# Performance work log

Hardware: AMD Instinct MI355X
Metric: run time of the kernel (lower is better)

Reference implementation:

```python
import jax, jax.numpy as jnp
import numpy as np

EPS = 1e-8  # torch CosineSimilarity eps


def _l2_normalize(x):
    n = jnp.sqrt(jnp.sum(x * x, axis=-1, keepdims=True))
    return x / jnp.maximum(n, EPS)


def setup_inputs() -> dict:
    key = jax.random.key(0)
    k1, k2, k3 = jax.random.split(key, 3)
    B, D, K = 4096, 1024, 256
    datapoints = jax.random.normal(k1, (B, D), dtype=jnp.float32)
    centroid = jax.random.normal(k2, (K, D), dtype=jnp.float32)
    batch_cos_sim = jax.random.normal(k3, (B, B), dtype=jnp.float32)
    return {"datapoints": datapoints, "centroid": centroid, "batch_cos_sim": batch_cos_sim}


def reference(datapoints, centroid, batch_cos_sim):
    # --- _clustering: cosine similarity datapoints[B,D] vs centroid[K,D] (temp=1) ---
    dn = _l2_normalize(datapoints)                       # [B, D]
    cn = _l2_normalize(centroid)                         # [K, D]
    intra_cos_sim = jnp.einsum('bd,kd->bk', dn, cn)      # [B, K]
    dp_index = jnp.argmax(intra_cos_sim, axis=-1)        # [B]

    # --- _intra_class_adjacency: one-hot matmul, zero diagonal ---
    onehot = jax.nn.one_hot(dp_index, centroid.shape[0], dtype=jnp.float32)  # [B, K]
    dp_cluster = jnp.einsum('bk,ck->bc', onehot, onehot)                      # [B, B]
    B = datapoints.shape[0]
    dp_cluster = dp_cluster * (1.0 - jnp.eye(B, dtype=dp_cluster.dtype))
    index_dp = onehot.T.astype(jnp.int32)                # [K, B]

    # --- gather centroid each datapoint belongs to ---
    dp_centroid = centroid[dp_index]                     # [B, D]

    # --- provide_hard_negative: top-2, take 2nd-best centroid ---
    top_vals, top_idx = jax.lax.top_k(intra_cos_sim, 2)  # [B, 2]
    hard_neg_index = top_idx[:, 1]                       # [B]
    hard_negative = centroid[hard_neg_index]             # [B, D]

    return (intra_cos_sim, dp_index, dp_cluster, index_dp, dp_centroid,
            hard_negative, hard_neg_index, top_vals[:, 1])
```

## Files before the change

kernel.cpp:

```cpp
#include <hip/hip_runtime.h>
#include <hip/hip_bf16.h>
#include <math.h>

#define B_N 4096
#define D_N 1024
#define K_N 256
#define NSTEP 32

typedef __attribute__((ext_vector_type(8))) short bf16x8;
typedef __attribute__((ext_vector_type(8))) unsigned short u16x8;
typedef __attribute__((ext_vector_type(4))) float f32x4;
typedef __attribute__((ext_vector_type(4))) float f32x4v;
typedef __attribute__((ext_vector_type(4))) int   i32x4;

static constexpr float K_EPS = 1e-8f;

static __device__ __forceinline__ unsigned short f32_to_bf16_rne(float f) {
    unsigned x = __builtin_bit_cast(unsigned, f);
    unsigned r = (x + 0x7FFFu + ((x >> 16) & 1u)) >> 16;
    return (unsigned short)r;
}
static __device__ __forceinline__ float bf16_bits_to_f32(unsigned short h) {
    unsigned x = ((unsigned)h) << 16;
    return __builtin_bit_cast(float, x);
}
static __device__ __forceinline__ void cvt8(
    float e0, float e1, float e2, float e3,
    float e4, float e5, float e6, float e7, u16x8& hv, u16x8& lv)
{
    ushort h0=f32_to_bf16_rne(e0), h1=f32_to_bf16_rne(e1),
           h2=f32_to_bf16_rne(e2), h3=f32_to_bf16_rne(e3),
           h4=f32_to_bf16_rne(e4), h5=f32_to_bf16_rne(e5),
           h6=f32_to_bf16_rne(e6), h7=f32_to_bf16_rne(e7);
    hv = (u16x8){h0,h1,h2,h3,h4,h5,h6,h7};
    lv = (u16x8){f32_to_bf16_rne(e0 - bf16_bits_to_f32(h0)),
                 f32_to_bf16_rne(e1 - bf16_bits_to_f32(h1)),
                 f32_to_bf16_rne(e2 - bf16_bits_to_f32(h2)),
                 f32_to_bf16_rne(e3 - bf16_bits_to_f32(h3)),
                 f32_to_bf16_rne(e4 - bf16_bits_to_f32(h4)),
                 f32_to_bf16_rne(e5 - bf16_bits_to_f32(h5)),
                 f32_to_bf16_rne(e6 - bf16_bits_to_f32(h6)),
                 f32_to_bf16_rne(e7 - bf16_bits_to_f32(h7))};
}

__global__ __launch_bounds__(256) void kcent_kernel(
    const float* __restrict__ cent,
    ushort* __restrict__ phi, ushort* __restrict__ plo)
{
    int n   = blockIdx.x;
    int tid = threadIdx.x;
    float4 v = reinterpret_cast<const float4*>(cent + (size_t)n * D_N)[tid];
    float s = v.x * v.x + v.y * v.y + v.z * v.z + v.w * v.w;
    #pragma unroll
    for (int o = 32; o > 0; o >>= 1) s += __shfl_down(s, o);
    __shared__ float red[4];
    __shared__ float s_inv;
    if ((tid & 63) == 0) red[tid >> 6] = s;
    __syncthreads();
    if (tid == 0) {
        float t = red[0] + red[1] + red[2] + red[3];
        s_inv = 1.0f / fmaxf(sqrtf(t), K_EPS);
    }
    __syncthreads();
    float inv = s_inv;
    float e[4] = {v.x * inv, v.y * inv, v.z * inv, v.w * inv};
    ushort h4[4], l4[4];
    #pragma unroll
    for (int j = 0; j < 4; ++j) {
        ushort h = f32_to_bf16_rne(e[j]);
        float lo = e[j] - bf16_bits_to_f32(h);
        h4[j] = h;
        l4[j] = f32_to_bf16_rne(lo);
    }
    int nt = n >> 4, lr = n & 15;
    int k8 = tid >> 1, half = tid & 1;
    int t  = k8 >> 2, lg = k8 & 3;
    size_t chunk = (size_t)(nt * 32 + t) * 64 + lg * 16 + lr;
    *reinterpret_cast<ushort4*>(phi + chunk * 8 + half * 4) =
        make_ushort4(h4[0], h4[1], h4[2], h4[3]);
    *reinterpret_cast<ushort4*>(plo + chunk * 8 + half * 4) =
        make_ushort4(l4[0], l4[1], l4[2], l4[3]);
}

__global__ __launch_bounds__(1024) void kmain_kernel(
    const float* __restrict__ dp, const float* __restrict__ cent,
    const ushort* __restrict__ phi, const ushort* __restrict__ plo,
    float* __restrict__ out_sims, float* __restrict__ out_dpidx,
    float* __restrict__ out_hnidx, float* __restrict__ out_top1,
    float* __restrict__ out_dpcent, float* __restrict__ out_hneg,
    int* __restrict__ ws_dpidx)
{
    __shared__ ushort AhL[16 * 1024];
    __shared__ ushort AlL[16 * 1024];
    __shared__ float  simsL[16 * 256];
    int tid  = threadIdx.x;
    int lane = tid & 63;
    int w    = tid >> 6;
    int lr   = lane & 15;
    int lg   = lane >> 4;
    int brow = blockIdx.x * 16;

    const ushort* bh = phi + (size_t)w * 32 * 512 + (size_t)lane * 8;
    const ushort* bl = plo + (size_t)w * 32 * 512 + (size_t)lane * 8;

    #define LBF(t, H, L)                                                  \
        H = *reinterpret_cast<const bf16x8*>(bh + (size_t)(t) * 512);     \
        L = *reinterpret_cast<const bf16x8*>(bl + (size_t)(t) * 512);

    bf16x8 h0,l0,h1,l1,h2,l2,h3,l3,h4,l4,h5,l5,h6,l6,h7,l7;
    LBF(0,h0,l0) LBF(1,h1,l1) LBF(2,h2,l2) LBF(3,h3,l3)
    LBF(4,h4,l4) LBF(5,h5,l5) LBF(6,h6,l6) LBF(7,h7,l7)

    {
        const f32x4v* r4 = reinterpret_cast<const f32x4v*>(
            dp + (size_t)(brow + w) * D_N);
        f32x4v a0 = __builtin_nontemporal_load(r4 + lane*4+0);
        f32x4v a1 = __builtin_nontemporal_load(r4 + lane*4+1);
        f32x4v a2 = __builtin_nontemporal_load(r4 + lane*4+2);
        f32x4v a3 = __builtin_nontemporal_load(r4 + lane*4+3);
        float s = a0[0]*a0[0] + a0[1]*a0[1] + a0[2]*a0[2] + a0[3]*a0[3]
                + a1[0]*a1[0] + a1[1]*a1[1] + a1[2]*a1[2] + a1[3]*a1[3]
                + a2[0]*a2[0] + a2[1]*a2[1] + a2[2]*a2[2] + a2[3]*a2[3]
                + a3[0]*a3[0] + a3[1]*a3[1] + a3[2]*a3[2] + a3[3]*a3[3];
        #pragma unroll
        for (int o = 1; o < 64; o <<= 1) s += __shfl_xor(s, o);
        float inv = 1.0f / fmaxf(sqrtf(s), K_EPS);
        u16x8 hv, lv;
        cvt8(a0[0]*inv, a0[1]*inv, a0[2]*inv, a0[3]*inv,
             a1[0]*inv, a1[1]*inv, a1[2]*inv, a1[3]*inv, hv, lv);
        int slot = (lane*2 + 0) ^ (w & 7);
        *reinterpret_cast<u16x8*>(&AhL[w*1024 + slot*8]) = hv;
        *reinterpret_cast<u16x8*>(&AlL[w*1024 + slot*8]) = lv;
        cvt8(a2[0]*inv, a2[1]*inv, a2[2]*inv, a2[3]*inv,
             a3[0]*inv, a3[1]*inv, a3[2]*inv, a3[3]*inv, hv, lv);
        slot = (lane*2 + 1) ^ (w & 7);
        *reinterpret_cast<u16x8*>(&AhL[w*1024 + slot*8]) = hv;
        *reinterpret_cast<u16x8*>(&AlL[w*1024 + slot*8]) = lv;
    }
    __syncthreads();

    f32x4 acc = {};
    const char* AhC = (const char*)AhL;
    const char* AlC = (const char*)AlL;
    auto step = [&](int t, bf16x8 hb, bf16x8 lb) {
        unsigned ca = (unsigned)((4*t + lg) ^ (lr & 7));
        unsigned ao = (unsigned)lr * 2048u + ca * 16u;
        bf16x8 ah = *reinterpret_cast<const bf16x8*>(AhC + ao);
        bf16x8 al = *reinterpret_cast<const bf16x8*>(AlC + ao);
        acc = __builtin_amdgcn_mfma_f32_16x16x32_bf16(ah, hb, acc, 0, 0, 0);
        acc = __builtin_amdgcn_mfma_f32_16x16x32_bf16(ah, lb, acc, 0, 0, 0);
        acc = __builtin_amdgcn_mfma_f32_16x16x32_bf16(al, hb, acc, 0, 0, 0);
    };
    #pragma unroll 1
    for (int t = 0; t < NSTEP; t += 8) {
        step(t + 0, h0, l0); if (t +  8 < NSTEP) { LBF(t +  8, h0, l0) }
        step(t + 1, h1, l1); if (t +  9 < NSTEP) { LBF(t +  9, h1, l1) }
        step(t + 2, h2, l2); if (t + 10 < NSTEP) { LBF(t + 10, h2, l2) }
        step(t + 3, h3, l3); if (t + 11 < NSTEP) { LBF(t + 11, h3, l3) }
        step(t + 4, h4, l4); if (t + 12 < NSTEP) { LBF(t + 12, h4, l4) }
        step(t + 5, h5, l5); if (t + 13 < NSTEP) { LBF(t + 13, h5, l5) }
        step(t + 6, h6, l6); if (t + 14 < NSTEP) { LBF(t + 14, h6, l6) }
        step(t + 7, h7, l7); if (t + 15 < NSTEP) { LBF(t + 15, h7, l7) }
    }
    #undef LBF

    #pragma unroll
    for (int r = 0; r < 4; ++r)
        simsL[(lg*4 + r) * K_N + w*16 + lr] = acc[r];
    __syncthreads();

    {
        f32x4v c = *reinterpret_cast<const f32x4v*>(&simsL[w * K_N + lane * 4]);
        int row = brow + w;
        __builtin_nontemporal_store(c,
            reinterpret_cast<f32x4v*>(&out_sims[(size_t)row * K_N + lane * 4]));
        float v1b = c[0]; int i1 = lane * 4;
        float v2b = -INFINITY; int i2 = 0;
        {
            float vals[3] = {c[1], c[2], c[3]};
            #pragma unroll
            for (int j = 0; j < 3; ++j) {
                float val = vals[j]; int idx = lane * 4 + j + 1;
                if (val > v1b) { v2b = v1b; i2 = i1; v1b = val; i1 = idx; }
                else if (val > v2b) { v2b = val; i2 = idx; }
            }
        }
        #pragma unroll
        for (int o = 1; o < 64; o <<= 1) {
            float ov1 = __shfl_xor(v1b, o);
            float ov2 = __shfl_xor(v2b, o);
            int   oi1 = __shfl_xor(i1, o);
            int   oi2 = __shfl_xor(i2, o);
            if (ov1 > v1b || (ov1 == v1b && oi1 < i1)) {
                float nv2; int ni2;
                if (v1b > ov2 || (v1b == ov2 && i1 < oi2)) { nv2 = v1b; ni2 = i1; }
                else { nv2 = ov2; ni2 = oi2; }
                v1b = ov1; i1 = oi1; v2b = nv2; i2 = ni2;
            } else if (ov1 > v2b || (ov1 == v2b && oi1 < i2)) {
                v2b = ov1; i2 = oi1;
            }
        }
        const f32x4v* cent4 = reinterpret_cast<const f32x4v*>(cent);
        #pragma unroll
        for (int q = 0; q < 4; ++q) {
            f32x4v g1 = cent4[(size_t)i1 * 256 + q * 64 + lane];
            f32x4v g2 = cent4[(size_t)i2 * 256 + q * 64 + lane];
            __builtin_nontemporal_store(g1,
                reinterpret_cast<f32x4v*>(out_dpcent + (size_t)row * D_N) + q*64 + lane);
            __builtin_nontemporal_store(g2,
                reinterpret_cast<f32x4v*>(out_hneg + (size_t)row * D_N) + q*64 + lane);
        }
        if (lane == 0) {
            out_dpidx[row] = (float)i1;
            out_hnidx[row] = (float)i2;
            out_top1[row]  = v2b;
            ws_dpidx[row]  = i1;
        }
    }
}

__global__ __launch_bounds__(256) void kclust_kernel(
    const int* __restrict__ dpidx,
    float* __restrict__ out_cluster, float* __restrict__ out_indexdp)
{
    int bid = blockIdx.x;
    int tid = threadIdx.x;
    const i32x4* dpi4 = reinterpret_cast<const i32x4*>(dpidx);
    if (bid < B_N) {
        int i = bid;
        int me = dpidx[i];
        float* dst = out_cluster + (size_t)i * B_N;
        #pragma unroll
        for (int q = 0; q < 4; ++q) {
            int j = q * 1024 + tid * 4;
            i32x4 ix = dpi4[j >> 2];
            f32x4v v;
            v[0] = (ix[0] == me && (j + 0) != i) ? 1.0f : 0.0f;
            v[1] = (ix[1] == me && (j + 1) != i) ? 1.0f : 0.0f;
            v[2] = (ix[2] == me && (j + 2) != i) ? 1.0f : 0.0f;
            v[3] = (ix[3] == me && (j + 3) != i) ? 1.0f : 0.0f;
            __builtin_nontemporal_store(v, reinterpret_cast<f32x4v*>(dst + j));
        }
    } else {
        int k = bid - B_N;
        float* dst = out_indexdp + (size_t)k * B_N;
        #pragma unroll
        for (int q = 0; q < 4; ++q) {
            int j = q * 1024 + tid * 4;
            i32x4 ix = dpi4[j >> 2];
            f32x4v v;
            v[0] = (ix[0] == k) ? 1.0f : 0.0f;
            v[1] = (ix[1] == k) ? 1.0f : 0.0f;
            v[2] = (ix[2] == k) ? 1.0f : 0.0f;
            v[3] = (ix[3] == k) ? 1.0f : 0.0f;
            __builtin_nontemporal_store(v, reinterpret_cast<f32x4v*>(dst + j));
        }
    }
}

extern "C" void kernel_launch(void* const* d_in, const int* in_sizes, int n_in,
                              void* d_out, int out_size, void* d_ws, size_t ws_size,
                              hipStream_t stream)
{
    const float* dp   = (const float*)d_in[0];
    const float* cent = (const float*)d_in[1];
    float* out = (float*)d_out;

    float* o_sims   = out;
    float* o_dpidx  = out + 1048576;
    float* o_clust  = out + 1052672;
    float* o_idxdp  = out + 17829888;
    float* o_dpcent = out + 18878464;
    float* o_hneg   = out + 23072768;
    float* o_hnidx  = out + 27267072;
    float* o_top1   = out + 27271168;

    char* ws = (char*)d_ws;
    ushort* phi  = (ushort*)ws;
    ushort* plo  = (ushort*)(ws + (512u << 10));
    int*    widx = (int*)(ws + (1u << 20));

    hipLaunchKernelGGL(kcent_kernel, dim3(K_N), dim3(256), 0, stream,
                       cent, phi, plo);
    hipLaunchKernelGGL(kmain_kernel, dim3(B_N / 16), dim3(1024), 0, stream,
                       dp, cent, phi, plo,
                       o_sims, o_dpidx, o_hnidx, o_top1,
                       o_dpcent, o_hneg, widx);
    hipLaunchKernelGGL(kclust_kernel, dim3(B_N + K_N), dim3(256), 0, stream,
                       widx, o_clust, o_idxdp);
}
```

Baseline: 44.41 us.

## Process 32 datapoint rows per block to reuse centroid fragments across two tiles

```diff
diff --git a/kernel.cpp b/kernel.cpp
--- a/kernel.cpp
+++ b/kernel.cpp
@@ -90,15 +90,15 @@
     float* __restrict__ out_dpcent, float* __restrict__ out_hneg,
     int* __restrict__ ws_dpidx)
 {
-    __shared__ ushort AhL[16 * 1024];
-    __shared__ ushort AlL[16 * 1024];
-    __shared__ float  simsL[16 * 256];
+    __shared__ ushort AhL[32 * 1024];
+    __shared__ ushort AlL[32 * 1024];
+    float* simsL = (float*)AhL;
     int tid  = threadIdx.x;
     int lane = tid & 63;
     int w    = tid >> 6;
     int lr   = lane & 15;
     int lg   = lane >> 4;
-    int brow = blockIdx.x * 16;
+    int brow = blockIdx.x * 32;
 
     const ushort* bh = phi + (size_t)w * 32 * 512 + (size_t)lane * 8;
     const ushort* bl = plo + (size_t)w * 32 * 512 + (size_t)lane * 8;
@@ -111,9 +111,11 @@
     LBF(0,h0,l0) LBF(1,h1,l1) LBF(2,h2,l2) LBF(3,h3,l3)
     LBF(4,h4,l4) LBF(5,h5,l5) LBF(6,h6,l6) LBF(7,h7,l7)
 
-    {
+    #pragma unroll
+    for (int rloc = 0; rloc < 2; ++rloc) {
+        int row_l = w * 2 + rloc;
         const f32x4v* r4 = reinterpret_cast<const f32x4v*>(
-            dp + (size_t)(brow + w) * D_N);
+            dp + (size_t)(brow + row_l) * D_N);
         f32x4v a0 = __builtin_nontemporal_load(r4 + lane*4+0);
         f32x4v a1 = __builtin_nontemporal_load(r4 + lane*4+1);
         f32x4v a2 = __builtin_nontemporal_load(r4 + lane*4+2);
@@ -128,28 +130,34 @@
         u16x8 hv, lv;
         cvt8(a0[0]*inv, a0[1]*inv, a0[2]*inv, a0[3]*inv,
              a1[0]*inv, a1[1]*inv, a1[2]*inv, a1[3]*inv, hv, lv);
-        int slot = (lane*2 + 0) ^ (w & 7);
-        *reinterpret_cast<u16x8*>(&AhL[w*1024 + slot*8]) = hv;
-        *reinterpret_cast<u16x8*>(&AlL[w*1024 + slot*8]) = lv;
+        int slot = (lane*2 + 0) ^ (row_l & 7);
+        *reinterpret_cast<u16x8*>(&AhL[row_l*1024 + slot*8]) = hv;
+        *reinterpret_cast<u16x8*>(&AlL[row_l*1024 + slot*8]) = lv;
         cvt8(a2[0]*inv, a2[1]*inv, a2[2]*inv, a2[3]*inv,
              a3[0]*inv, a3[1]*inv, a3[2]*inv, a3[3]*inv, hv, lv);
-        slot = (lane*2 + 1) ^ (w & 7);
-        *reinterpret_cast<u16x8*>(&AhL[w*1024 + slot*8]) = hv;
-        *reinterpret_cast<u16x8*>(&AlL[w*1024 + slot*8]) = lv;
-    }
-    __syncthreads();
-
-    f32x4 acc = {};
+        slot = (lane*2 + 1) ^ (row_l & 7);
+        *reinterpret_cast<u16x8*>(&AhL[row_l*1024 + slot*8]) = hv;
+        *reinterpret_cast<u16x8*>(&AlL[row_l*1024 + slot*8]) = lv;
+    }
+    __syncthreads();
+
+    f32x4 acc0 = {}, acc1 = {};
     const char* AhC = (const char*)AhL;
     const char* AlC = (const char*)AlL;
     auto step = [&](int t, bf16x8 hb, bf16x8 lb) {
         unsigned ca = (unsigned)((4*t + lg) ^ (lr & 7));
-        unsigned ao = (unsigned)lr * 2048u + ca * 16u;
-        bf16x8 ah = *reinterpret_cast<const bf16x8*>(AhC + ao);
-        bf16x8 al = *reinterpret_cast<const bf16x8*>(AlC + ao);
-        acc = __builtin_amdgcn_mfma_f32_16x16x32_bf16(ah, hb, acc, 0, 0, 0);
-        acc = __builtin_amdgcn_mfma_f32_16x16x32_bf16(ah, lb, acc, 0, 0, 0);
-        acc = __builtin_amdgcn_mfma_f32_16x16x32_bf16(al, hb, acc, 0, 0, 0);
+        unsigned ao0 = (unsigned)lr * 2048u + ca * 16u;
+        unsigned ao1 = (unsigned)(16 + lr) * 2048u + ca * 16u;
+        bf16x8 ah0 = *reinterpret_cast<const bf16x8*>(AhC + ao0);
+        bf16x8 al0 = *reinterpret_cast<const bf16x8*>(AlC + ao0);
+        bf16x8 ah1 = *reinterpret_cast<const bf16x8*>(AhC + ao1);
+        bf16x8 al1 = *reinterpret_cast<const bf16x8*>(AlC + ao1);
+        acc0 = __builtin_amdgcn_mfma_f32_16x16x32_bf16(ah0, hb, acc0, 0, 0, 0);
+        acc0 = __builtin_amdgcn_mfma_f32_16x16x32_bf16(ah0, lb, acc0, 0, 0, 0);
+        acc0 = __builtin_amdgcn_mfma_f32_16x16x32_bf16(al0, hb, acc0, 0, 0, 0);
+        acc1 = __builtin_amdgcn_mfma_f32_16x16x32_bf16(ah1, hb, acc1, 0, 0, 0);
+        acc1 = __builtin_amdgcn_mfma_f32_16x16x32_bf16(ah1, lb, acc1, 0, 0, 0);
+        acc1 = __builtin_amdgcn_mfma_f32_16x16x32_bf16(al1, hb, acc1, 0, 0, 0);
     };
     #pragma unroll 1
     for (int t = 0; t < NSTEP; t += 8) {
@@ -164,14 +172,19 @@
     }
     #undef LBF
 
-    #pragma unroll
-    for (int r = 0; r < 4; ++r)
-        simsL[(lg*4 + r) * K_N + w*16 + lr] = acc[r];
-    __syncthreads();
-
-    {
-        f32x4v c = *reinterpret_cast<const f32x4v*>(&simsL[w * K_N + lane * 4]);
-        int row = brow + w;
+    __syncthreads();
+    #pragma unroll
+    for (int r = 0; r < 4; ++r) {
+        simsL[(lg*4 + r) * K_N + w*16 + lr]        = acc0[r];
+        simsL[(16 + lg*4 + r) * K_N + w*16 + lr]   = acc1[r];
+    }
+    __syncthreads();
+
+    #pragma unroll
+    for (int rloc = 0; rloc < 2; ++rloc) {
+        int row_l = w * 2 + rloc;
+        int row   = brow + row_l;
+        f32x4v c = *reinterpret_cast<const f32x4v*>(&simsL[row_l * K_N + lane * 4]);
         __builtin_nontemporal_store(c,
             reinterpret_cast<f32x4v*>(&out_sims[(size_t)row * K_N + lane * 4]));
         float v1b = c[0]; int i1 = lane * 4;
@@ -282,7 +295,7 @@
 
     hipLaunchKernelGGL(kcent_kernel, dim3(K_N), dim3(256), 0, stream,
                        cent, phi, plo);
-    hipLaunchKernelGGL(kmain_kernel, dim3(B_N / 16), dim3(1024), 0, stream,
+    hipLaunchKernelGGL(kmain_kernel, dim3(B_N / 32), dim3(1024), 0, stream,
                        dp, cent, phi, plo,
                        o_sims, o_dpidx, o_hnidx, o_top1,
                        o_dpcent, o_hneg, widx);
```

New measurement: 49.47 us. 1.11x slower.
